# Kernel optimization log

Hardware: AMD Instinct MI355X
Metric: run time of the kernel (lower is better)

Reference implementation:

```python
import jax, jax.numpy as jnp
import numpy as np

B, T, IN, H, L, OUT, PRED, FN = 512, 96, 64, 512, 2, 1, 24, 32


def setup_inputs() -> dict:
    key = jax.random.key(0)
    ks = jax.random.split(key, 12)
    sc = 0.02
    n = lambda i, shape: jax.random.normal(ks[i], shape, jnp.float32) * sc
    return {
        "x": jax.random.normal(ks[0], (B, T, IN), jnp.float32),
        "station_id": jax.random.randint(ks[1], (B,), 0, 26, jnp.int32),
        "W_hidden": n(2, (H, IN)), "b_hidden": jnp.zeros((H,), jnp.float32),
        "embed": n(3, (26, H)),
        "W_ih": n(4, (L, 4 * H, H)), "W_hh": n(5, (L, 4 * H, H)),
        "b_ih": jnp.zeros((L, 4 * H), jnp.float32), "b_hh": jnp.zeros((L, 4 * H), jnp.float32),
        "conv_W": n(6, (FN, T - 1)), "conv_b": jnp.zeros((FN,), jnp.float32),
        "W1": n(7, (FN, H)), "b1": jnp.zeros((FN,), jnp.float32),
        "W2": n(8, (H, H + FN)), "b2": jnp.zeros((H,), jnp.float32),
        "W_out": n(9, (T * OUT, H)), "b_out": jnp.zeros((T * OUT,), jnp.float32),
    }


def _lstm(xc, W_ih, W_hh, b_ih, b_hh):
    # xc: [B, T, H]; multi-layer LSTM, PyTorch gate order i,f,g,o
    n_layers = W_ih.shape[0]
    h0 = jnp.zeros((n_layers, xc.shape[0], W_hh.shape[-1]), xc.dtype)

    def step(carry, xt):
        h, c = carry  # [L, B, H]
        inp = xt
        hs, cs = [], []
        for l in range(n_layers):
            g = inp @ W_ih[l].T + h[l] @ W_hh[l].T + b_ih[l] + b_hh[l]
            i, f, gg, o = jnp.split(g, 4, axis=-1)
            cn = jax.nn.sigmoid(f) * c[l] + jax.nn.sigmoid(i) * jnp.tanh(gg)
            hn = jax.nn.sigmoid(o) * jnp.tanh(cn)
            hs.append(hn); cs.append(cn)
            inp = hn
        return (jnp.stack(hs), jnp.stack(cs)), inp  # emit last-layer h

    _, outs = jax.lax.scan(step, (h0, h0), jnp.swapaxes(xc, 0, 1))
    return jnp.swapaxes(outs, 0, 1)  # [B, T, H] last-layer hidden states


def reference(x, station_id, W_hidden, b_hidden, embed, W_ih, W_hh, b_ih, b_hh,
              conv_W, conv_b, W1, b1, W2, b2, W_out, b_out):
    b, t, _ = x.shape
    hdim = W_hidden.shape[0]
    fn = conv_W.shape[0]
    xc = jax.nn.relu(x @ W_hidden.T + b_hidden)
    xc = xc + embed[station_id][:, None, :]
    hs_seq = _lstm(xc, W_ih, W_hh, b_ih, b_hh)          # [B, T, H]
    Hmat = jax.nn.relu(hs_seq[:, :-1, :])                # [B, T-1, H]
    htt = hs_seq[:, -1, :]                               # [B, H]
    # Conv2d(1, FN, (T-1, 1)) over [B,1,T-1,H] == contraction over time
    conv = jax.nn.relu(jnp.einsum('bth,ft->bfh', Hmat, conv_W) + conv_b[None, :, None])
    # original does .view(-1, feat_size, filter_num): raw reshape, not transpose
    feat = conv.reshape(b, hdim, fn)                     # [B, H, FN]
    w = (htt @ W1.T + b1)[:, None, :]                    # [B, 1, FN]
    alpha = jax.nn.sigmoid(jnp.sum(feat * w, axis=2))    # [B, H]
    v = jnp.sum(alpha[:, :, None] * feat, axis=1)        # [B, FN]
    new_ht = jnp.concatenate([htt, v], axis=1) @ W2.T + b2
    ypred = (new_ht @ W_out.T + b_out)[:, -PRED * OUT:]
    return ypred
```

## Files before the change

### kernel.cpp

```cpp
#include <hip/hip_runtime.h>
#include <math.h>

namespace {

constexpr int B = 512, T = 96, IN = 64, H = 512, G4 = 2048;
constexpr int FN = 32, KC = 544, NPRED = 24, TM1 = T - 1;
constexpr int BH = B * H;

typedef __attribute__((ext_vector_type(8))) short s8v;
typedef __attribute__((ext_vector_type(16))) float f16v;

__device__ __forceinline__ float sigf(float x) { return 1.0f / (1.0f + __expf(-x)); }
__device__ __forceinline__ float tanhfast(float x) {
  x = fminf(fmaxf(x, -15.f), 15.f);
  float e = __expf(2.0f * x);
  return (e - 1.0f) / (e + 1.0f);
}
__device__ __forceinline__ unsigned short bf16_rne(float f) {
  unsigned u = __float_as_uint(f);
  u += 0x7fffu + ((u >> 16) & 1u);
  return (unsigned short)(u >> 16);
}
__device__ __forceinline__ void split8(const float4& x, const float4& y, s8v& hi, s8v& lo) {
  float vs[8] = {x.x, x.y, x.z, x.w, y.x, y.y, y.z, y.w};
#pragma unroll
  for (int j = 0; j < 8; ++j) {
    unsigned ub = __float_as_uint(vs[j]);
    hi[j] = (short)(ub >> 16);
    lo[j] = (short)bf16_rne(vs[j] - __uint_as_float(ub & 0xffff0000u));
  }
}

__global__ __launch_bounds__(256) void k_xc(
    const float* __restrict__ x, const int* __restrict__ sid,
    const float* __restrict__ Wh, const float* __restrict__ bh,
    const float* __restrict__ emb, float* __restrict__ planes) {
  constexpr int RWS = 64;
  int gid = blockIdx.x;
  int half = gid & 1;
  int row0 = (gid >> 1) * RWS;
  int tid = threadIdx.x;
  int h = half * 256 + tid;
  __shared__ float sx[RWS][IN];
  {
    const float4* xsrc = (const float4*)(x + (size_t)row0 * IN);
    float4* sdst = (float4*)(&sx[0][0]);
    for (int i = tid; i < RWS * IN / 4; i += 256) sdst[i] = xsrc[i];
  }
  float4 w[16];
  const float* wr = Wh + (size_t)h * IN;
#pragma unroll
  for (int j = 0; j < 16; ++j) w[j] = *(const float4*)(wr + j * 4);
  float b0 = bh[h];
  const float* ep = emb + h;
  __syncthreads();
#pragma unroll 2
  for (int r = 0; r < RWS; ++r) {
    float a0 = b0, a1 = 0.f, a2 = 0.f, a3 = 0.f;
#pragma unroll
    for (int j = 0; j < 16; ++j) {
      float4 xv = *(const float4*)(&sx[r][j * 4]);
      a0 = fmaf(xv.x, w[j].x, a0);
      a1 = fmaf(xv.y, w[j].y, a1);
      a2 = fmaf(xv.z, w[j].z, a2);
      a3 = fmaf(xv.w, w[j].w, a3);
    }
    float acc = (a0 + a1) + (a2 + a3);
    int row = row0 + r;
    int bb = row / T, t = row % T;
    float v = fmaxf(acc, 0.f) + ep[(size_t)sid[bb] * H];
    planes[((size_t)t * B + bb) * H + h] = v;
  }
}

__global__ __launch_bounds__(256) void k_wswz(
    const float* __restrict__ Wih, const float* __restrict__ Whh,
    short* __restrict__ WFhi, short* __restrict__ WFlo) {
  int g = blockIdx.x * 256 + threadIdx.x;
  int lane = g & 63;
  int fi = g >> 6;
  int nt = fi & 3, kt = (fi >> 2) & 63, ng = (fi >> 8) & 15, layer = fi >> 12;
  int row = nt * H + ng * 32 + (lane & 31);
  int kk = kt * 16 + (lane >> 5) * 8;
  const float* src = (kk < H) ? (Wih + ((size_t)layer * G4 + row) * H + kk)
                              : (Whh + ((size_t)layer * G4 + row) * H + (kk - H));
  float4 f0 = *(const float4*)src, f1 = *(const float4*)(src + 4);
  s8v hi, lo;
  split8(f0, f1, hi, lo);
  size_t o = (size_t)fi * 512 + lane * 8;
  *(s8v*)(WFhi + o) = hi;
  *(s8v*)(WFlo + o) = lo;
}

__global__ __launch_bounds__(256, 1) void k_step(
    int tt, float* __restrict__ planes, const short* __restrict__ WFhi,
    const short* __restrict__ WFlo, short* __restrict__ hFhi,
    short* __restrict__ hFlo, const float* __restrict__ bih,
    const float* __restrict__ bhh, float* __restrict__ c0,
    float* __restrict__ c1) {
  int gid = blockIdx.x;
  int xcd = gid & 7;
  int u = gid >> 3;
  int combo = xcd * 4 + (u & 3);
  int layer = combo >> 4;
  if (layer ? (tt == 0) : (tt == T)) return;
  int ng = combo & 15;
  int b0 = (u >> 2) * 64;
  int step = layer ? (tt - 1) : tt;
  int tid = threadIdx.x, lane = tid & 63, wk = tid >> 6;
  int l31 = lane & 31, lh = lane >> 5;

  __shared__ float comb[4][4][32][32];

  const float* bi = bih + (size_t)layer * G4;
  const float* bh2 = bhh + (size_t)layer * G4;
  float* cbuf = layer ? c1 : c0;

  int rpar = (step - 1) & 1;
  const float* xbase = nullptr;
  const short *abhi = nullptr, *ablo = nullptr;
  if (layer == 0 && wk < 2) {
    xbase = planes + (size_t)step * BH + (size_t)(b0 + l31) * H + wk * 256 + lh * 8;
  } else {
    int src = (layer == 0) ? 0 : ((wk < 2) ? 0 : 1);
    int par = (layer == 0) ? rpar : ((wk < 2) ? (step & 1) : rpar);
    int kk0 = wk * 16 - ((layer == 0 || wk >= 2) ? 32 : 0);
    size_t o = ((((size_t)src * 2 + par) * 32 + kk0) * H + (b0 + l31)) * 16 + lh * 8;
    abhi = hFhi + o;
    ablo = hFlo + o;
  }

  float bias[4];
#pragma unroll
  for (int nt = 0; nt < 4; ++nt) {
    int r = nt * H + ng * 32 + l31;
    bias[nt] = bi[r] + bh2[r];
  }

  const size_t wstep = 4 * 512;
  const size_t wbase0 = ((size_t)(layer * 16 + ng) * 64 + wk * 16) * wstep + (size_t)lane * 8;
  const size_t astep = (size_t)H * 16;

  f16v acc[2][4];
#pragma unroll
  for (int rt = 0; rt < 2; ++rt)
#pragma unroll
    for (int nt = 0; nt < 4; ++nt)
#pragma unroll
      for (int e = 0; e < 16; ++e) acc[rt][nt][e] = 0.f;

  s8v a0h0, a0l0, a0h1, a0l1, b0h0, b0h1, b0h2, b0h3, b0l0, b0l1, b0l2, b0l3;
  s8v a1h0, a1l0, a1h1, a1l1, b1h0, b1h1, b1h2, b1h3, b1l0, b1l1, b1l2, b1l3;
  s8v a2h0, a2l0, a2h1, a2l1, b2h0, b2h1, b2h2, b2h3, b2l0, b2l1, b2l2, b2l3;

#define LOADW_(kq, bh0, bh1, bh2, bh3, bl0, bl1, bl2, bl3)          \
  {                                                                 \
    size_t wo = wbase0 + (size_t)(kq) * wstep;                      \
    bh0 = *(const s8v*)(WFhi + wo);                                 \
    bh1 = *(const s8v*)(WFhi + wo + 512);                           \
    bh2 = *(const s8v*)(WFhi + wo + 1024);                          \
    bh3 = *(const s8v*)(WFhi + wo + 1536);                          \
    bl0 = *(const s8v*)(WFlo + wo);                                 \
    bl1 = *(const s8v*)(WFlo + wo + 512);                           \
    bl2 = *(const s8v*)(WFlo + wo + 1024);                          \
    bl3 = *(const s8v*)(WFlo + wo + 1536);                          \
  }
#define LOADA_(kq, ah0, al0, ah1, al1)                              \
  {                                                                 \
    if (xbase) {                                                    \
      const float* ap = xbase + (kq) * 16;                          \
      float4 f0 = *(const float4*)ap, f1 = *(const float4*)(ap + 4);\
      split8(f0, f1, ah0, al0);                                     \
      const float* aq = ap + 32 * H;                                \
      float4 g0 = *(const float4*)aq, g1 = *(const float4*)(aq + 4);\
      split8(g0, g1, ah1, al1);                                     \
    } else {                                                        \
      const short* ph = abhi + (size_t)(kq) * astep;                \
      const short* pl = ablo + (size_t)(kq) * astep;                \
      ah0 = *(const s8v*)(ph);                                      \
      al0 = *(const s8v*)(pl);                                      \
      ah1 = *(const s8v*)(ph + 512);                                \
      al1 = *(const s8v*)(pl + 512);                                \
    }                                                               \
  }
#define MFMA3R_(rt, ah, al, bh0, bh1, bh2, bh3, bl0, bl1, bl2, bl3)                        \
  {                                                                                        \
    acc[rt][0] = __builtin_amdgcn_mfma_f32_32x32x16_bf16(ah, bh0, acc[rt][0], 0, 0, 0);    \
    acc[rt][1] = __builtin_amdgcn_mfma_f32_32x32x16_bf16(ah, bh1, acc[rt][1], 0, 0, 0);    \
    acc[rt][2] = __builtin_amdgcn_mfma_f32_32x32x16_bf16(ah, bh2, acc[rt][2], 0, 0, 0);    \
    acc[rt][3] = __builtin_amdgcn_mfma_f32_32x32x16_bf16(ah, bh3, acc[rt][3], 0, 0, 0);    \
    acc[rt][0] = __builtin_amdgcn_mfma_f32_32x32x16_bf16(ah, bl0, acc[rt][0], 0, 0, 0);    \
    acc[rt][1] = __builtin_amdgcn_mfma_f32_32x32x16_bf16(ah, bl1, acc[rt][1], 0, 0, 0);    \
    acc[rt][2] = __builtin_amdgcn_mfma_f32_32x32x16_bf16(ah, bl2, acc[rt][2], 0, 0, 0);    \
    acc[rt][3] = __builtin_amdgcn_mfma_f32_32x32x16_bf16(ah, bl3, acc[rt][3], 0, 0, 0);    \
    acc[rt][0] = __builtin_amdgcn_mfma_f32_32x32x16_bf16(al, bh0, acc[rt][0], 0, 0, 0);    \
    acc[rt][1] = __builtin_amdgcn_mfma_f32_32x32x16_bf16(al, bh1, acc[rt][1], 0, 0, 0);    \
    acc[rt][2] = __builtin_amdgcn_mfma_f32_32x32x16_bf16(al, bh2, acc[rt][2], 0, 0, 0);    \
    acc[rt][3] = __builtin_amdgcn_mfma_f32_32x32x16_bf16(al, bh3, acc[rt][3], 0, 0, 0);    \
  }
#define MFMA6_(ah0, al0, ah1, al1, bh0, bh1, bh2, bh3, bl0, bl1, bl2, bl3)  \
  {                                                                         \
    MFMA3R_(0, ah0, al0, bh0, bh1, bh2, bh3, bl0, bl1, bl2, bl3);           \
    MFMA3R_(1, ah1, al1, bh0, bh1, bh2, bh3, bl0, bl1, bl2, bl3);           \
  }

  LOADA_(0, a0h0, a0l0, a0h1, a0l1);
  LOADW_(0, b0h0, b0h1, b0h2, b0h3, b0l0, b0l1, b0l2, b0l3);
  LOADA_(1, a1h0, a1l0, a1h1, a1l1);
  LOADW_(1, b1h0, b1h1, b1h2, b1h3, b1l0, b1l1, b1l2, b1l3);
  LOADA_(2, a2h0, a2l0, a2h1, a2l1);
  LOADW_(2, b2h0, b2h1, b2h2, b2h3, b2l0, b2l1, b2l2, b2l3);
#pragma unroll 1
  for (int kp = 0; kp < 5; ++kp) {
    int kq = kp * 3;
    MFMA6_(a0h0, a0l0, a0h1, a0l1, b0h0, b0h1, b0h2, b0h3, b0l0, b0l1, b0l2, b0l3);
    LOADA_(kq + 3, a0h0, a0l0, a0h1, a0l1);
    LOADW_(kq + 3, b0h0, b0h1, b0h2, b0h3, b0l0, b0l1, b0l2, b0l3);
    MFMA6_(a1h0, a1l0, a1h1, a1l1, b1h0, b1h1, b1h2, b1h3, b1l0, b1l1, b1l2, b1l3);
    if (kp < 4) {
      LOADA_(kq + 4, a1h0, a1l0, a1h1, a1l1);
      LOADW_(kq + 4, b1h0, b1h1, b1h2, b1h3, b1l0, b1l1, b1l2, b1l3);
    }
    MFMA6_(a2h0, a2l0, a2h1, a2l1, b2h0, b2h1, b2h2, b2h3, b2l0, b2l1, b2l2, b2l3);
    if (kp < 4) {
      LOADA_(kq + 5, a2h0, a2l0, a2h1, a2l1);
      LOADW_(kq + 5, b2h0, b2h1, b2h2, b2h3, b2l0, b2l1, b2l2, b2l3);
    }
  }
  MFMA6_(a0h0, a0l0, a0h1, a0l1, b0h0, b0h1, b0h2, b0h3, b0l0, b0l1, b0l2, b0l3);
#undef LOADW_
#undef LOADA_
#undef MFMA3R_
#undef MFMA6_

#pragma unroll
  for (int rt = 0; rt < 2; ++rt) {
    if (rt) __syncthreads();
#pragma unroll
    for (int nt = 0; nt < 4; ++nt)
#pragma unroll
      for (int r = 0; r < 16; ++r) {
        int row = (r & 3) + 8 * (r >> 2) + 4 * lh;
        comb[nt][wk][row][l31] = acc[rt][nt][r];
      }
    __syncthreads();
    int b0p = b0 + rt * 32;
#pragma unroll
    for (int rr = 0; rr < 4; ++rr) {
      int r = wk * 4 + rr;
      int row = (r & 3) + 8 * (r >> 2) + 4 * lh;
      float g[4];
#pragma unroll
      for (int nt = 0; nt < 4; ++nt) {
        float p0 = comb[nt][0][row][l31];
        float p1 = comb[nt][1][row][l31];
        float p2 = comb[nt][2][row][l31];
        float p3 = comb[nt][3][row][l31];
        g[nt] = (p0 + p1) + (p2 + p3) + bias[nt];
      }
      size_t coff = (size_t)(b0p + row) * H + ng * 32 + l31;
      float cp = cbuf[coff];
      float cn = sigf(g[1]) * cp + sigf(g[0]) * tanhfast(g[2]);
      float hn = sigf(g[3]) * tanhfast(cn);
      cbuf[coff] = cn;
      int brow = b0p + row;
      int hcol = ng * 32 + l31;
      size_t o = ((((size_t)layer * 2 + (step & 1)) * 32 + (hcol >> 4)) * H + brow) * 16 + (hcol & 15);
      unsigned ub = __float_as_uint(hn);
      hFhi[o] = (short)(ub >> 16);
      hFlo[o] = (short)bf16_rne(hn - __uint_as_float(ub & 0xffff0000u));
      if (layer) planes[(size_t)step * BH + (size_t)brow * H + hcol] = hn;
    }
  }
}

__global__ __launch_bounds__(256) void k_conv(
    const float* __restrict__ hs, const float* __restrict__ cW,
    const float* __restrict__ cb, float* __restrict__ feat) {
  int b = blockIdx.x >> 2;
  int h0 = (blockIdx.x & 3) * 128;
  int tid = threadIdx.x;
  __shared__ float sW[TM1][FN];
  for (int i = tid; i < TM1 * FN; i += 256) sW[i >> 5][i & 31] = cW[(i & 31) * TM1 + (i >> 5)];
  __syncthreads();
  int hl = tid & 127, fg = (tid >> 7) * 16;
  float acc[16];
#pragma unroll
  for (int j = 0; j < 16; ++j) acc[j] = cb[fg + j];
  const float* hp = hs + (size_t)b * H + h0 + hl;
  for (int t = 0; t < TM1; ++t) {
    float v = fmaxf(hp[(size_t)t * BH], 0.f);
#pragma unroll
    for (int j = 0; j < 16; ++j) acc[j] = fmaf(v, sW[t][fg + j], acc[j]);
  }
#pragma unroll
  for (int j = 0; j < 16; ++j)
    feat[(size_t)b * (FN * H) + (size_t)(fg + j) * H + h0 + hl] = fmaxf(acc[j], 0.f);
}

__global__ __launch_bounds__(256) void k_attn(
    const float* __restrict__ hs, const float* __restrict__ feat,
    const float* __restrict__ W1, const float* __restrict__ b1,
    const float* __restrict__ W2, const float* __restrict__ b2,
    const float* __restrict__ Wout, const float* __restrict__ bout,
    float* __restrict__ out) {
  int b = blockIdx.x, tid = threadIdx.x;
  __shared__ float sh[H], sa[H], snew[H], sw[FN], sv[FN], red[256];
  const float* htt = hs + (size_t)(T - 1) * BH + (size_t)b * H;
  for (int i = tid; i < H; i += 256) sh[i] = htt[i];
  __syncthreads();
  {
    int f = tid >> 3, sl = tid & 7;
    const float* w1 = W1 + (size_t)f * H;
    float p = 0.f;
    for (int k = sl * 64; k < sl * 64 + 64; ++k) p = fmaf(sh[k], w1[k], p);
    p += __shfl_xor(p, 1); p += __shfl_xor(p, 2); p += __shfl_xor(p, 4);
    if (sl == 0) sw[f] = p + b1[f];
  }
  __syncthreads();
  const float* fb = feat + (size_t)b * (FN * H);
  for (int i = tid; i < H; i += 256) {
    const float* fr = fb + (size_t)i * FN;
    float p = 0.f;
#pragma unroll
    for (int j = 0; j < FN; j += 4) {
      float4 fv = *(const float4*)(fr + j);
      p = fmaf(fv.x, sw[j], p);
      p = fmaf(fv.y, sw[j + 1], p);
      p = fmaf(fv.z, sw[j + 2], p);
      p = fmaf(fv.w, sw[j + 3], p);
    }
    sa[i] = sigf(p);
  }
  __syncthreads();
  {
    int j = tid & 31, isl = tid >> 5;
    float p = 0.f;
    for (int i = isl * 64; i < isl * 64 + 64; ++i) p = fmaf(sa[i], fb[(size_t)i * FN + j], p);
    red[tid] = p;
  }
  __syncthreads();
  if (tid < 128) red[tid] += red[tid + 128];
  __syncthreads();
  if (tid < 64) red[tid] += red[tid + 64];
  __syncthreads();
  if (tid < 32) sv[tid] = red[tid] + red[tid + 32];
  __syncthreads();
  for (int h = tid; h < H; h += 256) {
    const float* w2 = W2 + (size_t)h * KC;
    float p = b2[h];
#pragma unroll 4
    for (int k = 0; k < H; k += 4) {
      float4 wv = *(const float4*)(w2 + k);
      float4 shv = *(const float4*)(sh + k);
      p = fmaf(shv.x, wv.x, p);
      p = fmaf(shv.y, wv.y, p);
      p = fmaf(shv.z, wv.z, p);
      p = fmaf(shv.w, wv.w, p);
    }
#pragma unroll
    for (int j = 0; j < FN; j += 4) {
      float4 wv = *(const float4*)(w2 + H + j);
      p = fmaf(sv[j], wv.x, p);
      p = fmaf(sv[j + 1], wv.y, p);
      p = fmaf(sv[j + 2], wv.z, p);
      p = fmaf(sv[j + 3], wv.w, p);
    }
    snew[h] = p;
  }
  __syncthreads();
  if (tid < NPRED * 8) {
    int p = tid >> 3, sl = tid & 7;
    const float* wo = Wout + (size_t)(T - NPRED + p) * H;
    float sacc = 0.f;
    for (int k = sl * 64; k < sl * 64 + 64; ++k) sacc = fmaf(snew[k], wo[k], sacc);
    sacc += __shfl_xor(sacc, 1); sacc += __shfl_xor(sacc, 2); sacc += __shfl_xor(sacc, 4);
    if (sl == 0) out[(size_t)b * NPRED + p] = sacc + bout[T - NPRED + p];
  }
}

}

extern "C" void kernel_launch(void* const* d_in, const int* in_sizes, int n_in,
                              void* d_out, int out_size, void* d_ws, size_t ws_size,
                              hipStream_t stream) {
  const float* x    = (const float*)d_in[0];
  const int*   sid  = (const int*)d_in[1];
  const float* Wh   = (const float*)d_in[2];
  const float* bh   = (const float*)d_in[3];
  const float* emb  = (const float*)d_in[4];
  const float* Wih  = (const float*)d_in[5];
  const float* Whh  = (const float*)d_in[6];
  const float* bih  = (const float*)d_in[7];
  const float* bhh  = (const float*)d_in[8];
  const float* cW   = (const float*)d_in[9];
  const float* cb   = (const float*)d_in[10];
  const float* W1   = (const float*)d_in[11];
  const float* b1   = (const float*)d_in[12];
  const float* W2   = (const float*)d_in[13];
  const float* b2   = (const float*)d_in[14];
  const float* Wout = (const float*)d_in[15];
  const float* bout = (const float*)d_in[16];
  float* out = (float*)d_out;

  constexpr size_t HFE = (size_t)2 * 2 * 32 * H * 16;
  float* planes = (float*)d_ws;
  short* WFhi = (short*)(planes + (size_t)T * BH);
  short* WFlo = WFhi + (size_t)8192 * 512;
  short* hFhi = WFlo + (size_t)8192 * 512;
  short* hFlo = hFhi + HFE;
  float* cst = (float*)(hFlo + HFE);
  float* c0 = cst;
  float* c1 = cst + BH;
  float* feat = c1 + BH;
  size_t need = (size_t)T * BH * 4 + (size_t)8192 * 512 * 2 * 2 + HFE * 2 * 2 +
                2 * (size_t)BH * 4 + (size_t)B * FN * H * 4;
  if (ws_size < need) return;

  hipMemsetAsync(hFhi, 0, HFE * 2 * 2 + 2 * (size_t)BH * 4, stream);
  k_xc<<<(B * T / 64) * 2, 256, 0, stream>>>(x, sid, Wh, bh, emb, planes);
  k_wswz<<<2048, 256, 0, stream>>>(Wih, Whh, WFhi, WFlo);

  for (int tt = 0; tt <= T; ++tt)
    k_step<<<256, 256, 0, stream>>>(tt, planes, WFhi, WFlo, hFhi, hFlo, bih, bhh, c0, c1);

  k_conv<<<B * 4, 256, 0, stream>>>(planes, cW, cb, feat);
  k_attn<<<B, 256, 0, stream>>>(planes, feat, W1, b1, W2, b2, Wout, bout, out);
}
```

Baseline: 2.324 ms.

## Stage LSTM step operands through LDS with async global_load_lds pipeline

Adds a new LSTM step kernel that streams pre-swizzled weight and activation tiles into a 4-deep LDS ring using global_load_lds. Loads are split across waves and guarded by vmcnt waits and barriers, and the K dimension is split across warps. A new pre-pass converts the layer-0 input planes into swizzled bf16 hi/lo form, so the per-step fp32 split work is removed. The hidden-state layout changes to match the new tiles. The aim is better overlap of memory latency with MFMA work in the latency-bound recurrent steps, at the cost of extra workspace and a swizzle pass. The old path stays as a fallback when the workspace is too small.

```diff
diff --git a/kernel.cpp b/kernel.cpp
--- a/kernel.cpp
+++ b/kernel.cpp
@@ -29,6 +29,11 @@
     hi[j] = (short)(ub >> 16);
     lo[j] = (short)bf16_rne(vs[j] - __uint_as_float(ub & 0xffff0000u));
   }
+}
+__device__ __forceinline__ void gll16(const short* g, short* l) {
+  __builtin_amdgcn_global_load_lds(
+      (__attribute__((address_space(1))) void*)(void*)g,
+      (__attribute__((address_space(3))) void*)l, 16, 0, 0);
 }
 
 __global__ __launch_bounds__(256) void k_xc(
@@ -92,7 +97,196 @@
   *(s8v*)(WFlo + o) = lo;
 }
 
-__global__ __launch_bounds__(256, 1) void k_step(
+__global__ __launch_bounds__(256) void k_xswz(
+    const float* __restrict__ planes, short* __restrict__ xFhi,
+    short* __restrict__ xFlo) {
+  int g = blockIdx.x * 256 + threadIdx.x;
+  int lane = g & 63;
+  int fi = g >> 6;
+  int rt = fi & 1, kt = (fi >> 1) & 31, btile = (fi >> 6) & 7, t = fi >> 9;
+  int row = btile * 64 + rt * 32 + (lane & 31);
+  int kk = kt * 16 + (lane >> 5) * 8;
+  const float* src = planes + ((size_t)t * B + row) * H + kk;
+  float4 f0 = *(const float4*)src, f1 = *(const float4*)(src + 4);
+  s8v hi, lo;
+  split8(f0, f1, hi, lo);
+  size_t o = (size_t)fi * 512 + lane * 8;
+  *(s8v*)(xFhi + o) = hi;
+  *(s8v*)(xFlo + o) = lo;
+}
+
+__global__ __launch_bounds__(256, 1) void k_step3(
+    int tt, float* __restrict__ planes, const short* __restrict__ WFhi,
+    const short* __restrict__ WFlo, short* __restrict__ hFhi,
+    short* __restrict__ hFlo, const short* __restrict__ xFhi,
+    const short* __restrict__ xFlo, const float* __restrict__ bih,
+    const float* __restrict__ bhh, float* __restrict__ c0,
+    float* __restrict__ c1) {
+  int gid = blockIdx.x;
+  int xcd = gid & 7;
+  int u = gid >> 3;
+  int combo = xcd * 4 + (u & 3);
+  int layer = combo >> 4;
+  if (layer ? (tt == 0) : (tt == T)) return;
+  int ng = combo & 15;
+  int btile = u >> 2;
+  int b0 = btile * 64;
+  int step = layer ? (tt - 1) : tt;
+  int tid = threadIdx.x, lane = tid & 63, wk = tid >> 6;
+  int l31 = lane & 31, lh = lane >> 5;
+
+  __shared__ __align__(16) short sbuf[4][2][12][512];
+  __shared__ float comb[4][2][32][32];
+
+  int rpar = (step - 1) & 1;
+  const short *pa0h, *pa0l, *pa1h, *pa1l;
+  if (layer == 0) {
+    size_t xo = ((size_t)step * 8 + btile) * 32 * 1024;
+    pa0h = xFhi + xo;
+    pa0l = xFlo + xo;
+    size_t ho = (((size_t)0 * 2 + rpar) * 8 + btile) * 32 * 1024;
+    pa1h = hFhi + ho;
+    pa1l = hFlo + ho;
+  } else {
+    size_t h0o = (((size_t)0 * 2 + (step & 1)) * 8 + btile) * 32 * 1024;
+    pa0h = hFhi + h0o;
+    pa0l = hFlo + h0o;
+    size_t h1o = (((size_t)1 * 2 + rpar) * 8 + btile) * 32 * 1024;
+    pa1h = hFhi + h1o;
+    pa1l = hFlo + h1o;
+  }
+  const size_t wofs = (size_t)(layer * 16 + ng) * 64 * 2048;
+
+  const float* bi = bih + (size_t)layer * G4;
+  const float* bh2 = bhh + (size_t)layer * G4;
+  float* cbuf = layer ? c1 : c0;
+  float bias[4];
+#pragma unroll
+  for (int nt = 0; nt < 4; ++nt) {
+    int r = nt * H + ng * 32 + l31;
+    bias[nt] = bi[r] + bh2[r];
+  }
+  asm volatile("s_waitcnt vmcnt(0)" ::: "memory");
+
+  f16v acc0, acc1, acc2, acc3;
+#pragma unroll
+  for (int e = 0; e < 16; ++e) acc0[e] = acc1[e] = acc2[e] = acc3[e] = 0.f;
+
+#define STAGE(pp)                                                                \
+  {                                                                              \
+    short* lb_ = &sbuf[(pp) & 3][wk >> 1][0][0];                                 \
+    int kt_ = 2 * (pp) + (wk >> 1);                                              \
+    const short* wsh_ = WFhi + wofs + (size_t)kt_ * 2048 + lane * 8;             \
+    const short* wsl_ = WFlo + wofs + (size_t)kt_ * 2048 + lane * 8;             \
+    if ((wk & 1) == 0) {                                                         \
+      gll16(wsh_, lb_);                                                          \
+      gll16(wsh_ + 512, lb_ + 512);                                              \
+      gll16(wsh_ + 1024, lb_ + 1024);                                            \
+      gll16(wsh_ + 1536, lb_ + 1536);                                            \
+      gll16(wsl_, lb_ + 4 * 512);                                                \
+      gll16(wsl_ + 512, lb_ + 5 * 512);                                          \
+    } else {                                                                     \
+      const short* ah_ =                                                         \
+          ((kt_ < 32) ? pa0h + (size_t)kt_ * 1024 : pa1h + (size_t)(kt_ - 32) * 1024) + lane * 8; \
+      const short* al_ =                                                         \
+          ((kt_ < 32) ? pa0l + (size_t)kt_ * 1024 : pa1l + (size_t)(kt_ - 32) * 1024) + lane * 8; \
+      gll16(wsl_ + 1024, lb_ + 6 * 512);                                         \
+      gll16(wsl_ + 1536, lb_ + 7 * 512);                                         \
+      gll16(ah_, lb_ + 8 * 512);                                                 \
+      gll16(ah_ + 512, lb_ + 9 * 512);                                           \
+      gll16(al_, lb_ + 10 * 512);                                                \
+      gll16(al_ + 512, lb_ + 11 * 512);                                          \
+    }                                                                            \
+  }
+
+#define MM(a_, b_, c_) c_ = __builtin_amdgcn_mfma_f32_32x32x16_bf16(a_, b_, c_, 0, 0, 0)
+#define COMPUTE(ph)                                        \
+  {                                                        \
+    const short* bu_ = &sbuf[(ph) & 3][0][0][0] + lane * 8;\
+    s8v wh0 = *(const s8v*)(bu_ + wk * 512);               \
+    s8v wl0 = *(const s8v*)(bu_ + (4 + wk) * 512);         \
+    s8v ah00 = *(const s8v*)(bu_ + 8 * 512);               \
+    s8v ah10 = *(const s8v*)(bu_ + 9 * 512);               \
+    s8v al00 = *(const s8v*)(bu_ + 10 * 512);              \
+    s8v al10 = *(const s8v*)(bu_ + 11 * 512);              \
+    s8v wh1 = *(const s8v*)(bu_ + (12 + wk) * 512);        \
+    s8v wl1 = *(const s8v*)(bu_ + (16 + wk) * 512);        \
+    s8v ah01 = *(const s8v*)(bu_ + 20 * 512);              \
+    s8v ah11 = *(const s8v*)(bu_ + 21 * 512);              \
+    s8v al01 = *(const s8v*)(bu_ + 22 * 512);              \
+    s8v al11 = *(const s8v*)(bu_ + 23 * 512);              \
+    MM(ah00, wh0, acc0); MM(ah10, wh0, acc1);              \
+    MM(ah01, wh1, acc2); MM(ah11, wh1, acc3);              \
+    MM(al00, wh0, acc0); MM(al10, wh0, acc1);              \
+    MM(al01, wh1, acc2); MM(al11, wh1, acc3);              \
+    MM(ah00, wl0, acc0); MM(ah10, wl0, acc1);              \
+    MM(ah01, wl1, acc2); MM(ah11, wl1, acc3);              \
+  }
+
+  STAGE(0);
+  STAGE(1);
+  STAGE(2);
+#pragma unroll 1
+  for (int ph = 0; ph < 29; ++ph) {
+    asm volatile("s_waitcnt vmcnt(12)" ::: "memory");
+    __builtin_amdgcn_s_barrier();
+    __builtin_amdgcn_sched_barrier(0);
+    STAGE(ph + 3);
+    COMPUTE(ph);
+  }
+  asm volatile("s_waitcnt vmcnt(12)" ::: "memory");
+  __builtin_amdgcn_s_barrier();
+  __builtin_amdgcn_sched_barrier(0);
+  COMPUTE(29);
+  asm volatile("s_waitcnt vmcnt(6)" ::: "memory");
+  __builtin_amdgcn_s_barrier();
+  __builtin_amdgcn_sched_barrier(0);
+  COMPUTE(30);
+  asm volatile("s_waitcnt vmcnt(0)" ::: "memory");
+  __builtin_amdgcn_s_barrier();
+  __builtin_amdgcn_sched_barrier(0);
+  COMPUTE(31);
+#undef STAGE
+#undef COMPUTE
+#undef MM
+
+#pragma unroll
+  for (int r = 0; r < 16; ++r) {
+    int row = (r & 3) + 8 * (r >> 2) + 4 * lh;
+    comb[wk][0][row][l31] = acc0[r] + acc2[r];
+    comb[wk][1][row][l31] = acc1[r] + acc3[r];
+  }
+  __syncthreads();
+
+  int col = tid & 31;
+  int rbase = (tid >> 5) * 8;
+#pragma unroll
+  for (int rr = 0; rr < 8; ++rr) {
+    int row = rbase + rr;
+    int r5 = row >> 5, r31 = row & 31;
+    float g0 = comb[0][r5][r31][col] + bias[0];
+    float g1 = comb[1][r5][r31][col] + bias[1];
+    float g2 = comb[2][r5][r31][col] + bias[2];
+    float g3 = comb[3][r5][r31][col] + bias[3];
+    int brow = b0 + row;
+    int hcol = ng * 32 + col;
+    size_t coff = (size_t)brow * H + hcol;
+    float cp = cbuf[coff];
+    float cn = sigf(g1) * cp + sigf(g0) * tanhfast(g2);
+    float hn = sigf(g3) * tanhfast(cn);
+    cbuf[coff] = cn;
+    int kt2 = hcol >> 4;
+    int lane2 = r31 | (((hcol >> 3) & 1) << 5);
+    size_t o = (((((size_t)layer * 2 + (step & 1)) * 8 + btile) * 32 + kt2) * 2 + r5) * 512 +
+               lane2 * 8 + (hcol & 7);
+    unsigned ub = __float_as_uint(hn);
+    hFhi[o] = (short)(ub >> 16);
+    hFlo[o] = (short)bf16_rne(hn - __uint_as_float(ub & 0xffff0000u));
+    if (layer) planes[(size_t)step * BH + (size_t)brow * H + hcol] = hn;
+  }
+}
+
+__global__ __launch_bounds__(256, 1) void k_step2(
     int tt, float* __restrict__ planes, const short* __restrict__ WFhi,
     const short* __restrict__ WFlo, short* __restrict__ hFhi,
     short* __restrict__ hFlo, const float* __restrict__ bih,
@@ -109,13 +303,10 @@
   int step = layer ? (tt - 1) : tt;
   int tid = threadIdx.x, lane = tid & 63, wk = tid >> 6;
   int l31 = lane & 31, lh = lane >> 5;
-
   __shared__ float comb[4][4][32][32];
-
   const float* bi = bih + (size_t)layer * G4;
   const float* bh2 = bhh + (size_t)layer * G4;
   float* cbuf = layer ? c1 : c0;
-
   int rpar = (step - 1) & 1;
   const float* xbase = nullptr;
   const short *abhi = nullptr, *ablo = nullptr;
@@ -129,18 +320,15 @@
     abhi = hFhi + o;
     ablo = hFlo + o;
   }
-
   float bias[4];
 #pragma unroll
   for (int nt = 0; nt < 4; ++nt) {
     int r = nt * H + ng * 32 + l31;
     bias[nt] = bi[r] + bh2[r];
   }
-
   const size_t wstep = 4 * 512;
   const size_t wbase0 = ((size_t)(layer * 16 + ng) * 64 + wk * 16) * wstep + (size_t)lane * 8;
   const size_t astep = (size_t)H * 16;
-
   f16v acc[2][4];
 #pragma unroll
   for (int rt = 0; rt < 2; ++rt)
@@ -148,11 +336,9 @@
     for (int nt = 0; nt < 4; ++nt)
 #pragma unroll
       for (int e = 0; e < 16; ++e) acc[rt][nt][e] = 0.f;
-
   s8v a0h0, a0l0, a0h1, a0l1, b0h0, b0h1, b0h2, b0h3, b0l0, b0l1, b0l2, b0l3;
   s8v a1h0, a1l0, a1h1, a1l1, b1h0, b1h1, b1h2, b1h3, b1l0, b1l1, b1l2, b1l3;
   s8v a2h0, a2l0, a2h1, a2l1, b2h0, b2h1, b2h2, b2h3, b2l0, b2l1, b2l2, b2l3;
-
 #define LOADW_(kq, bh0, bh1, bh2, bh3, bl0, bl1, bl2, bl3)          \
   {                                                                 \
     size_t wo = wbase0 + (size_t)(kq) * wstep;                      \
@@ -175,12 +361,12 @@
       float4 g0 = *(const float4*)aq, g1 = *(const float4*)(aq + 4);\
       split8(g0, g1, ah1, al1);                                     \
     } else {                                                        \
-      const short* ph = abhi + (size_t)(kq) * astep;                \
-      const short* pl = ablo + (size_t)(kq) * astep;                \
-      ah0 = *(const s8v*)(ph);                                      \
-      al0 = *(const s8v*)(pl);                                      \
-      ah1 = *(const s8v*)(ph + 512);                                \
-      al1 = *(const s8v*)(pl + 512);                                \
+      const short* ph_ = abhi + (size_t)(kq) * astep;               \
+      const short* pl_ = ablo + (size_t)(kq) * astep;               \
+      ah0 = *(const s8v*)(ph_);                                     \
+      al0 = *(const s8v*)(pl_);                                     \
+      ah1 = *(const s8v*)(ph_ + 512);                               \
+      al1 = *(const s8v*)(pl_ + 512);                               \
     }                                                               \
   }
 #define MFMA3R_(rt, ah, al, bh0, bh1, bh2, bh3, bl0, bl1, bl2, bl3)                        \
@@ -203,7 +389,6 @@
     MFMA3R_(0, ah0, al0, bh0, bh1, bh2, bh3, bl0, bl1, bl2, bl3);           \
     MFMA3R_(1, ah1, al1, bh0, bh1, bh2, bh3, bl0, bl1, bl2, bl3);           \
   }
-
   LOADA_(0, a0h0, a0l0, a0h1, a0l1);
   LOADW_(0, b0h0, b0h1, b0h2, b0h3, b0l0, b0l1, b0l2, b0l3);
   LOADA_(1, a1h0, a1l0, a1h1, a1l1);
@@ -232,7 +417,6 @@
 #undef LOADA_
 #undef MFMA3R_
 #undef MFMA6_
-
 #pragma unroll
   for (int rt = 0; rt < 2; ++rt) {
     if (rt) __syncthreads();
@@ -403,10 +587,38 @@
   const float* bout = (const float*)d_in[16];
   float* out = (float*)d_out;
 
-  constexpr size_t HFE = (size_t)2 * 2 * 32 * H * 16;
   float* planes = (float*)d_ws;
   short* WFhi = (short*)(planes + (size_t)T * BH);
   short* WFlo = WFhi + (size_t)8192 * 512;
+
+  constexpr size_t HF3 = (size_t)2 * 2 * 8 * 32 * 2 * 512;
+  constexpr size_t XFE = (size_t)T * 8 * 32 * 2 * 512;
+  size_t need3 = (size_t)T * BH * 4 + (size_t)8192 * 512 * 2 * 2 + HF3 * 2 * 2 +
+                 2 * (size_t)BH * 4 + XFE * 2 * 2;
+
+  if (ws_size >= need3) {
+    short* hFhi = WFlo + (size_t)8192 * 512;
+    short* hFlo = hFhi + HF3;
+    float* cst = (float*)(hFlo + HF3);
+    float* c0 = cst;
+    float* c1 = cst + BH;
+    short* xFhi = (short*)(c1 + BH);
+    short* xFlo = xFhi + XFE;
+    float* feat = (float*)xFhi;
+
+    hipMemsetAsync(hFhi, 0, HF3 * 2 * 2 + 2 * (size_t)BH * 4, stream);
+    k_xc<<<(B * T / 64) * 2, 256, 0, stream>>>(x, sid, Wh, bh, emb, planes);
+    k_wswz<<<2048, 256, 0, stream>>>(Wih, Whh, WFhi, WFlo);
+    k_xswz<<<12288, 256, 0, stream>>>(planes, xFhi, xFlo);
+    for (int tt = 0; tt <= T; ++tt)
+      k_step3<<<256, 256, 0, stream>>>(tt, planes, WFhi, WFlo, hFhi, hFlo, xFhi, xFlo,
+                                       bih, bhh, c0, c1);
+    k_conv<<<B * 4, 256, 0, stream>>>(planes, cW, cb, feat);
+    k_attn<<<B, 256, 0, stream>>>(planes, feat, W1, b1, W2, b2, Wout, bout, out);
+    return;
+  }
+
+  constexpr size_t HFE = (size_t)2 * 2 * 32 * H * 16;
   short* hFhi = WFlo + (size_t)8192 * 512;
   short* hFlo = hFhi + HFE;
   float* cst = (float*)(hFlo + HFE);
@@ -420,10 +632,8 @@
   hipMemsetAsync(hFhi, 0, HFE * 2 * 2 + 2 * (size_t)BH * 4, stream);
   k_xc<<<(B * T / 64) * 2, 256, 0, stream>>>(x, sid, Wh, bh, emb, planes);
   k_wswz<<<2048, 256, 0, stream>>>(Wih, Whh, WFhi, WFlo);
-
   for (int tt = 0; tt <= T; ++tt)
-    k_step<<<256, 256, 0, stream>>>(tt, planes, WFhi, WFlo, hFhi, hFlo, bih, bhh, c0, c1);
-
+    k_step2<<<256, 256, 0, stream>>>(tt, planes, WFhi, WFlo, hFhi, hFlo, bih, bhh, c0, c1);
   k_conv<<<B * 4, 256, 0, stream>>>(planes, cW, cb, feat);
   k_attn<<<B, 256, 0, stream>>>(planes, feat, W1, b1, W2, b2, Wout, bout, out);
 }
```

Measured after the change: 3.061 ms. 31.7% more time.

## Fuse LSTM timesteps into one persistent kernel with a grid-wide atomic barrier

Applied to the files above, without the earlier changes.

Replaces the 97 per-timestep kernel launches with a single persistent kernel that loops over time and synchronises all 256 blocks through a global atomic counter barrier. Cell state is kept in registers instead of being read from and written to global memory each step. The hidden state's hi and lo bf16 halves are packed into one 32-bit word, written with system-scope atomic stores and read with atomic 64-bit loads. This removes launch overhead and the global cell-state traffic, but it requires every block to be co-resident, and the spin barrier plus system-scope atomics add their own latency each step.

```diff
diff --git a/kernel.cpp b/kernel.cpp
--- a/kernel.cpp
+++ b/kernel.cpp
@@ -29,6 +29,25 @@
     hi[j] = (short)(ub >> 16);
     lo[j] = (short)bf16_rne(vs[j] - __uint_as_float(ub & 0xffff0000u));
   }
+}
+__device__ __forceinline__ void unpack8(unsigned long long q0, unsigned long long q1,
+                                        unsigned long long q2, unsigned long long q3,
+                                        s8v& hi, s8v& lo) {
+  unsigned u0 = (unsigned)q0, u1 = (unsigned)(q0 >> 32);
+  unsigned u2 = (unsigned)q1, u3 = (unsigned)(q1 >> 32);
+  unsigned u4 = (unsigned)q2, u5 = (unsigned)(q2 >> 32);
+  unsigned u6 = (unsigned)q3, u7 = (unsigned)(q3 >> 32);
+  uint4 hv, lv;
+  hv.x = (u0 >> 16) | (u1 & 0xffff0000u);
+  hv.y = (u2 >> 16) | (u3 & 0xffff0000u);
+  hv.z = (u4 >> 16) | (u5 & 0xffff0000u);
+  hv.w = (u6 >> 16) | (u7 & 0xffff0000u);
+  lv.x = (u0 & 0xffffu) | (u1 << 16);
+  lv.y = (u2 & 0xffffu) | (u3 << 16);
+  lv.z = (u4 & 0xffffu) | (u5 << 16);
+  lv.w = (u6 & 0xffffu) | (u7 << 16);
+  hi = __builtin_bit_cast(s8v, hv);
+  lo = __builtin_bit_cast(s8v, lv);
 }
 
 __global__ __launch_bounds__(256) void k_xc(
@@ -92,66 +111,70 @@
   *(s8v*)(WFlo + o) = lo;
 }
 
-__global__ __launch_bounds__(256, 1) void k_step(
-    int tt, float* __restrict__ planes, const short* __restrict__ WFhi,
-    const short* __restrict__ WFlo, short* __restrict__ hFhi,
-    short* __restrict__ hFlo, const float* __restrict__ bih,
-    const float* __restrict__ bhh, float* __restrict__ c0,
-    float* __restrict__ c1) {
+__global__ __launch_bounds__(256, 1) void k_lstm(
+    float* __restrict__ planes, const short* __restrict__ WFhi,
+    const short* __restrict__ WFlo, unsigned* __restrict__ hP,
+    const float* __restrict__ bih, const float* __restrict__ bhh,
+    unsigned* __restrict__ bar) {
   int gid = blockIdx.x;
   int xcd = gid & 7;
   int u = gid >> 3;
   int combo = xcd * 4 + (u & 3);
   int layer = combo >> 4;
-  if (layer ? (tt == 0) : (tt == T)) return;
   int ng = combo & 15;
-  int b0 = (u >> 2) * 64;
-  int step = layer ? (tt - 1) : tt;
+  int btile = u >> 2;
+  int b0 = btile * 64;
   int tid = threadIdx.x, lane = tid & 63, wk = tid >> 6;
   int l31 = lane & 31, lh = lane >> 5;
 
   __shared__ float comb[4][4][32][32];
 
-  const float* bi = bih + (size_t)layer * G4;
-  const float* bh2 = bhh + (size_t)layer * G4;
-  float* cbuf = layer ? c1 : c0;
-
-  int rpar = (step - 1) & 1;
-  const float* xbase = nullptr;
-  const short *abhi = nullptr, *ablo = nullptr;
-  if (layer == 0 && wk < 2) {
-    xbase = planes + (size_t)step * BH + (size_t)(b0 + l31) * H + wk * 256 + lh * 8;
-  } else {
-    int src = (layer == 0) ? 0 : ((wk < 2) ? 0 : 1);
-    int par = (layer == 0) ? rpar : ((wk < 2) ? (step & 1) : rpar);
-    int kk0 = wk * 16 - ((layer == 0 || wk >= 2) ? 32 : 0);
-    size_t o = ((((size_t)src * 2 + par) * 32 + kk0) * H + (b0 + l31)) * 16 + lh * 8;
-    abhi = hFhi + o;
-    ablo = hFlo + o;
-  }
-
   float bias[4];
 #pragma unroll
   for (int nt = 0; nt < 4; ++nt) {
-    int r = nt * H + ng * 32 + l31;
-    bias[nt] = bi[r] + bh2[r];
-  }
+    int r = layer * G4 + nt * H + ng * 32 + l31;
+    bias[nt] = bih[r] + bhh[r];
+  }
+  float creg[2][4];
+#pragma unroll
+  for (int rt = 0; rt < 2; ++rt)
+#pragma unroll
+    for (int rr = 0; rr < 4; ++rr) creg[rt][rr] = 0.f;
 
   const size_t wstep = 4 * 512;
   const size_t wbase0 = ((size_t)(layer * 16 + ng) * 64 + wk * 16) * wstep + (size_t)lane * 8;
-  const size_t astep = (size_t)H * 16;
-
-  f16v acc[2][4];
-#pragma unroll
-  for (int rt = 0; rt < 2; ++rt)
-#pragma unroll
-    for (int nt = 0; nt < 4; ++nt)
-#pragma unroll
-      for (int e = 0; e < 16; ++e) acc[rt][nt][e] = 0.f;
-
-  s8v a0h0, a0l0, a0h1, a0l1, b0h0, b0h1, b0h2, b0h3, b0l0, b0l1, b0l2, b0l3;
-  s8v a1h0, a1l0, a1h1, a1l1, b1h0, b1h1, b1h2, b1h3, b1l0, b1l1, b1l2, b1l3;
-  s8v a2h0, a2l0, a2h1, a2l1, b2h0, b2h1, b2h2, b2h3, b2l0, b2l1, b2l2, b2l3;
+  const bool use_x = (layer == 0) && (wk < 2);
+  const int srcA = (layer == 0) ? 0 : ((wk < 2) ? 0 : 1);
+  const int kt0 = wk * 16 - ((layer == 0 || wk >= 2) ? 32 : 0);
+
+#define LD8(p) __hip_atomic_load((const unsigned long long*)(p), __ATOMIC_RELAXED, __HIP_MEMORY_SCOPE_SYSTEM)
+
+#pragma unroll 1
+  for (int tt = 0; tt <= T; ++tt) {
+    bool active = layer ? (tt >= 1) : (tt < T);
+    int step = layer ? (tt - 1) : tt;
+    if (active) {
+      int rpar = (step - 1) & 1;
+      const float* xbase = nullptr;
+      const unsigned* hbase = nullptr;
+      if (use_x) {
+        xbase = planes + (size_t)step * BH + (size_t)(b0 + l31) * H + wk * 256 + lh * 8;
+      } else {
+        int par = (layer == 0) ? rpar : ((wk < 2) ? (step & 1) : rpar);
+        hbase = hP + ((((size_t)srcA * 2 + par) * 32 + kt0) * 512 + (b0 + l31)) * 16 + lh * 8;
+      }
+
+      f16v acc[2][4];
+#pragma unroll
+      for (int rt = 0; rt < 2; ++rt)
+#pragma unroll
+        for (int nt = 0; nt < 4; ++nt)
+#pragma unroll
+          for (int e = 0; e < 16; ++e) acc[rt][nt][e] = 0.f;
+
+      s8v a0h0, a0l0, a0h1, a0l1, b0h0, b0h1, b0h2, b0h3, b0l0, b0l1, b0l2, b0l3;
+      s8v a1h0, a1l0, a1h1, a1l1, b1h0, b1h1, b1h2, b1h3, b1l0, b1l1, b1l2, b1l3;
+      s8v a2h0, a2l0, a2h1, a2l1, b2h0, b2h1, b2h2, b2h3, b2l0, b2l1, b2l2, b2l3;
 
 #define LOADW_(kq, bh0, bh1, bh2, bh3, bl0, bl1, bl2, bl3)          \
   {                                                                 \
@@ -165,23 +188,24 @@
     bl2 = *(const s8v*)(WFlo + wo + 1024);                          \
     bl3 = *(const s8v*)(WFlo + wo + 1536);                          \
   }
-#define LOADA_(kq, ah0, al0, ah1, al1)                              \
-  {                                                                 \
-    if (xbase) {                                                    \
-      const float* ap = xbase + (kq) * 16;                          \
-      float4 f0 = *(const float4*)ap, f1 = *(const float4*)(ap + 4);\
-      split8(f0, f1, ah0, al0);                                     \
-      const float* aq = ap + 32 * H;                                \
-      float4 g0 = *(const float4*)aq, g1 = *(const float4*)(aq + 4);\
-      split8(g0, g1, ah1, al1);                                     \
-    } else {                                                        \
-      const short* ph = abhi + (size_t)(kq) * astep;                \
-      const short* pl = ablo + (size_t)(kq) * astep;                \
-      ah0 = *(const s8v*)(ph);                                      \
-      al0 = *(const s8v*)(pl);                                      \
-      ah1 = *(const s8v*)(ph + 512);                                \
-      al1 = *(const s8v*)(pl + 512);                                \
-    }                                                               \
+#define LOADA_(kq, ah0, al0, ah1, al1)                                           \
+  {                                                                              \
+    if (use_x) {                                                                 \
+      const float* ap = xbase + (kq) * 16;                                       \
+      float4 f0 = *(const float4*)ap, f1 = *(const float4*)(ap + 4);             \
+      split8(f0, f1, ah0, al0);                                                  \
+      const float* aq = ap + 32 * H;                                             \
+      float4 g0 = *(const float4*)aq, g1 = *(const float4*)(aq + 4);             \
+      split8(g0, g1, ah1, al1);                                                  \
+    } else {                                                                     \
+      const unsigned* hp0 = hbase + (size_t)(kq) * 8192;                         \
+      unsigned long long q0 = LD8(hp0), q1 = LD8(hp0 + 2);                       \
+      unsigned long long q2 = LD8(hp0 + 4), q3 = LD8(hp0 + 6);                   \
+      unsigned long long r0 = LD8(hp0 + 512), r1 = LD8(hp0 + 514);               \
+      unsigned long long r2 = LD8(hp0 + 516), r3 = LD8(hp0 + 518);               \
+      unpack8(q0, q1, q2, q3, ah0, al0);                                         \
+      unpack8(r0, r1, r2, r3, ah1, al1);                                         \
+    }                                                                            \
   }
 #define MFMA3R_(rt, ah, al, bh0, bh1, bh2, bh3, bl0, bl1, bl2, bl3)                        \
   {                                                                                        \
@@ -204,74 +228,90 @@
     MFMA3R_(1, ah1, al1, bh0, bh1, bh2, bh3, bl0, bl1, bl2, bl3);           \
   }
 
-  LOADA_(0, a0h0, a0l0, a0h1, a0l1);
-  LOADW_(0, b0h0, b0h1, b0h2, b0h3, b0l0, b0l1, b0l2, b0l3);
-  LOADA_(1, a1h0, a1l0, a1h1, a1l1);
-  LOADW_(1, b1h0, b1h1, b1h2, b1h3, b1l0, b1l1, b1l2, b1l3);
-  LOADA_(2, a2h0, a2l0, a2h1, a2l1);
-  LOADW_(2, b2h0, b2h1, b2h2, b2h3, b2l0, b2l1, b2l2, b2l3);
+      LOADA_(0, a0h0, a0l0, a0h1, a0l1);
+      LOADW_(0, b0h0, b0h1, b0h2, b0h3, b0l0, b0l1, b0l2, b0l3);
+      LOADA_(1, a1h0, a1l0, a1h1, a1l1);
+      LOADW_(1, b1h0, b1h1, b1h2, b1h3, b1l0, b1l1, b1l2, b1l3);
+      LOADA_(2, a2h0, a2l0, a2h1, a2l1);
+      LOADW_(2, b2h0, b2h1, b2h2, b2h3, b2l0, b2l1, b2l2, b2l3);
 #pragma unroll 1
-  for (int kp = 0; kp < 5; ++kp) {
-    int kq = kp * 3;
-    MFMA6_(a0h0, a0l0, a0h1, a0l1, b0h0, b0h1, b0h2, b0h3, b0l0, b0l1, b0l2, b0l3);
-    LOADA_(kq + 3, a0h0, a0l0, a0h1, a0l1);
-    LOADW_(kq + 3, b0h0, b0h1, b0h2, b0h3, b0l0, b0l1, b0l2, b0l3);
-    MFMA6_(a1h0, a1l0, a1h1, a1l1, b1h0, b1h1, b1h2, b1h3, b1l0, b1l1, b1l2, b1l3);
-    if (kp < 4) {
-      LOADA_(kq + 4, a1h0, a1l0, a1h1, a1l1);
-      LOADW_(kq + 4, b1h0, b1h1, b1h2, b1h3, b1l0, b1l1, b1l2, b1l3);
-    }
-    MFMA6_(a2h0, a2l0, a2h1, a2l1, b2h0, b2h1, b2h2, b2h3, b2l0, b2l1, b2l2, b2l3);
-    if (kp < 4) {
-      LOADA_(kq + 5, a2h0, a2l0, a2h1, a2l1);
-      LOADW_(kq + 5, b2h0, b2h1, b2h2, b2h3, b2l0, b2l1, b2l2, b2l3);
-    }
-  }
-  MFMA6_(a0h0, a0l0, a0h1, a0l1, b0h0, b0h1, b0h2, b0h3, b0l0, b0l1, b0l2, b0l3);
+      for (int kp = 0; kp < 5; ++kp) {
+        int kq = kp * 3;
+        MFMA6_(a0h0, a0l0, a0h1, a0l1, b0h0, b0h1, b0h2, b0h3, b0l0, b0l1, b0l2, b0l3);
+        LOADA_(kq + 3, a0h0, a0l0, a0h1, a0l1);
+        LOADW_(kq + 3, b0h0, b0h1, b0h2, b0h3, b0l0, b0l1, b0l2, b0l3);
+        MFMA6_(a1h0, a1l0, a1h1, a1l1, b1h0, b1h1, b1h2, b1h3, b1l0, b1l1, b1l2, b1l3);
+        if (kp < 4) {
+          LOADA_(kq + 4, a1h0, a1l0, a1h1, a1l1);
+          LOADW_(kq + 4, b1h0, b1h1, b1h2, b1h3, b1l0, b1l1, b1l2, b1l3);
+        }
+        MFMA6_(a2h0, a2l0, a2h1, a2l1, b2h0, b2h1, b2h2, b2h3, b2l0, b2l1, b2l2, b2l3);
+        if (kp < 4) {
+          LOADA_(kq + 5, a2h0, a2l0, a2h1, a2l1);
+          LOADW_(kq + 5, b2h0, b2h1, b2h2, b2h3, b2l0, b2l1, b2l2, b2l3);
+        }
+      }
+      MFMA6_(a0h0, a0l0, a0h1, a0l1, b0h0, b0h1, b0h2, b0h3, b0l0, b0l1, b0l2, b0l3);
 #undef LOADW_
 #undef LOADA_
 #undef MFMA3R_
 #undef MFMA6_
 
 #pragma unroll
-  for (int rt = 0; rt < 2; ++rt) {
-    if (rt) __syncthreads();
-#pragma unroll
-    for (int nt = 0; nt < 4; ++nt)
-#pragma unroll
-      for (int r = 0; r < 16; ++r) {
-        int row = (r & 3) + 8 * (r >> 2) + 4 * lh;
-        comb[nt][wk][row][l31] = acc[rt][nt][r];
+      for (int rt = 0; rt < 2; ++rt) {
+        if (rt) __syncthreads();
+#pragma unroll
+        for (int nt = 0; nt < 4; ++nt)
+#pragma unroll
+          for (int r = 0; r < 16; ++r) {
+            int row = (r & 3) + 8 * (r >> 2) + 4 * lh;
+            comb[nt][wk][row][l31] = acc[rt][nt][r];
+          }
+        __syncthreads();
+        int b0p = b0 + rt * 32;
+#pragma unroll
+        for (int rr = 0; rr < 4; ++rr) {
+          int r = wk * 4 + rr;
+          int row = (r & 3) + 8 * (r >> 2) + 4 * lh;
+          float g[4];
+#pragma unroll
+          for (int nt = 0; nt < 4; ++nt) {
+            float p0 = comb[nt][0][row][l31];
+            float p1 = comb[nt][1][row][l31];
+            float p2 = comb[nt][2][row][l31];
+            float p3 = comb[nt][3][row][l31];
+            g[nt] = (p0 + p1) + (p2 + p3) + bias[nt];
+          }
+          float cp = creg[rt][rr];
+          float cn = sigf(g[1]) * cp + sigf(g[0]) * tanhfast(g[2]);
+          float hn = sigf(g[3]) * tanhfast(cn);
+          creg[rt][rr] = cn;
+          int brow = b0p + row;
+          int hcol = ng * 32 + l31;
+          unsigned ub = __float_as_uint(hn);
+          unsigned hi16 = ub >> 16;
+          unsigned lo16 = (unsigned)bf16_rne(hn - __uint_as_float(ub & 0xffff0000u)) & 0xffffu;
+          unsigned pk = (hi16 << 16) | lo16;
+          size_t o = (((size_t)(layer * 2 + (step & 1)) * 32 + (hcol >> 4)) * 512 + brow) * 16 +
+                     (hcol & 15);
+          __hip_atomic_store(hP + o, pk, __ATOMIC_RELAXED, __HIP_MEMORY_SCOPE_SYSTEM);
+          if (layer) planes[(size_t)step * BH + (size_t)brow * H + hcol] = hn;
+        }
       }
-    __syncthreads();
-    int b0p = b0 + rt * 32;
-#pragma unroll
-    for (int rr = 0; rr < 4; ++rr) {
-      int r = wk * 4 + rr;
-      int row = (r & 3) + 8 * (r >> 2) + 4 * lh;
-      float g[4];
-#pragma unroll
-      for (int nt = 0; nt < 4; ++nt) {
-        float p0 = comb[nt][0][row][l31];
-        float p1 = comb[nt][1][row][l31];
-        float p2 = comb[nt][2][row][l31];
-        float p3 = comb[nt][3][row][l31];
-        g[nt] = (p0 + p1) + (p2 + p3) + bias[nt];
+    }
+
+    if (tt < T) {
+      __syncthreads();
+      if (tid == 0) {
+        __hip_atomic_fetch_add(bar, 1u, __ATOMIC_RELAXED, __HIP_MEMORY_SCOPE_SYSTEM);
+        unsigned tgt = 256u * (unsigned)(tt + 1);
+        while (__hip_atomic_load(bar, __ATOMIC_RELAXED, __HIP_MEMORY_SCOPE_SYSTEM) < tgt)
+          __builtin_amdgcn_s_sleep(2);
       }
-      size_t coff = (size_t)(b0p + row) * H + ng * 32 + l31;
-      float cp = cbuf[coff];
-      float cn = sigf(g[1]) * cp + sigf(g[0]) * tanhfast(g[2]);
-      float hn = sigf(g[3]) * tanhfast(cn);
-      cbuf[coff] = cn;
-      int brow = b0p + row;
-      int hcol = ng * 32 + l31;
-      size_t o = ((((size_t)layer * 2 + (step & 1)) * 32 + (hcol >> 4)) * H + brow) * 16 + (hcol & 15);
-      unsigned ub = __float_as_uint(hn);
-      hFhi[o] = (short)(ub >> 16);
-      hFlo[o] = (short)bf16_rne(hn - __uint_as_float(ub & 0xffff0000u));
-      if (layer) planes[(size_t)step * BH + (size_t)brow * H + hcol] = hn;
-    }
-  }
+      __syncthreads();
+    }
+  }
+#undef LD8
 }
 
 __global__ __launch_bounds__(256) void k_conv(
@@ -403,26 +443,22 @@
   const float* bout = (const float*)d_in[16];
   float* out = (float*)d_out;
 
-  constexpr size_t HFE = (size_t)2 * 2 * 32 * H * 16;
+  constexpr size_t HPU = (size_t)2 * 2 * 32 * 512 * 16;
   float* planes = (float*)d_ws;
   short* WFhi = (short*)(planes + (size_t)T * BH);
   short* WFlo = WFhi + (size_t)8192 * 512;
-  short* hFhi = WFlo + (size_t)8192 * 512;
-  short* hFlo = hFhi + HFE;
-  float* cst = (float*)(hFlo + HFE);
-  float* c0 = cst;
-  float* c1 = cst + BH;
-  float* feat = c1 + BH;
-  size_t need = (size_t)T * BH * 4 + (size_t)8192 * 512 * 2 * 2 + HFE * 2 * 2 +
-                2 * (size_t)BH * 4 + (size_t)B * FN * H * 4;
+  unsigned* hP = (unsigned*)(WFlo + (size_t)8192 * 512);
+  unsigned* bar = hP + HPU;
+  float* feat = (float*)(bar + 1024);
+  size_t need = (size_t)T * BH * 4 + (size_t)8192 * 512 * 2 * 2 + HPU * 4 + 4096 +
+                (size_t)B * FN * H * 4;
   if (ws_size < need) return;
 
-  hipMemsetAsync(hFhi, 0, HFE * 2 * 2 + 2 * (size_t)BH * 4, stream);
+  hipMemsetAsync(hP, 0, HPU * 4 + 4096, stream);
   k_xc<<<(B * T / 64) * 2, 256, 0, stream>>>(x, sid, Wh, bh, emb, planes);
   k_wswz<<<2048, 256, 0, stream>>>(Wih, Whh, WFhi, WFlo);
 
-  for (int tt = 0; tt <= T; ++tt)
-    k_step<<<256, 256, 0, stream>>>(tt, planes, WFhi, WFlo, hFhi, hFlo, bih, bhh, c0, c1);
+  k_lstm<<<256, 256, 0, stream>>>(planes, WFhi, WFlo, hP, bih, bhh, bar);
 
   k_conv<<<B * 4, 256, 0, stream>>>(planes, cW, cb, feat);
   k_attn<<<B, 256, 0, stream>>>(planes, feat, W1, b1, W2, b2, Wout, bout, out);
```

Result: slower. 2.758 ms (+18.7%).
